# Kernel tuning notes

Measured on AMD Instinct MI355X. Metric: run time of the kernel, lower is better.

The kernel has to match this reference:

```python
import jax, jax.numpy as jnp
import numpy as np

B, L, D, DA, NL = 32, 2048, 512, 512, 512

def setup_inputs() -> dict:
    key = jax.random.key(0)
    k1, k2, k3, k4 = jax.random.split(key, 4)
    std = 0.03
    return {
        "x": jax.random.normal(k1, (B, L, D), dtype=jnp.float32),
        "W1": jax.random.normal(k2, (DA, D), dtype=jnp.float32) * std,   # first_linears[0].weight [d_a, size]
        "W2": jax.random.normal(k3, (NL, DA), dtype=jnp.float32) * std,  # second_linears[0].weight [n_labels, d_a]
        "W3": jax.random.normal(k4, (NL, D), dtype=jnp.float32) * std,   # third_linears[0].weight [n_labels, size]
        "b3": jnp.zeros((NL,), dtype=jnp.float32),                        # third_linears[0].bias
    }

def reference(x, W1, W2, W3, b3):
    # weights = tanh(first_linear(x)) : [B, L, DA]
    w = jnp.tanh(jnp.einsum("bld,ad->bla", x, W1))
    # att logits : [B, L, NL]; softmax over seq dim (dim=1), then transpose -> [B, NL, L]
    att = jax.nn.softmax(jnp.einsum("bla,na->bln", w, W2), axis=1)
    att_weights = jnp.swapaxes(att, 1, 2)  # [B, NL, L]
    # context_vector = att_weights @ x : [B, NL, D]
    context_vector = jnp.einsum("bnl,bld->bnd", att_weights, x)
    # label-wise diagonal mul-sum-add: [B, NL]
    weighted_output = jnp.einsum("bnd,nd->bn", context_vector, W3) + b3
    return (context_vector, weighted_output, att_weights)
```

## Files before the change

kernel.cpp:

```cpp
#include <hip/hip_runtime.h>
#include <math.h>

#define BB 32
#define LL 2048
#define DD 512
#define DA_ 512
#define NL_ 512

typedef __bf16 bf16;
typedef __bf16 bf16x8 __attribute__((ext_vector_type(8)));
typedef __bf16 bf16x4 __attribute__((ext_vector_type(4)));
typedef float floatx4 __attribute__((ext_vector_type(4)));

__device__ __forceinline__ void dma16(const void* g, void* l) {
    __builtin_amdgcn_global_load_lds((__attribute__((address_space(1))) void*)g,
                                     (__attribute__((address_space(3))) void*)l,
                                     16, 0, 0);
}

__device__ __forceinline__ float fast_tanh(float x) {
    const float e = __expf(2.f * x);
    return 1.f - 2.f * __builtin_amdgcn_rcpf(e + 1.f);
}

template <bool AF, bool BF>
__device__ __forceinline__ void gemm_core(const void* Ap_, const void* Bp_,
                                          int K, int lda, int ldb,
                                          floatx4 acc[4][4])
{
    __shared__ bf16 As[128 * 32];
    __shared__ bf16 Bs[128 * 32];
    const int tid = threadIdx.x;
    const int lane = tid & 63, wv = tid >> 6;
    const int wr = wv >> 1, wc = wv & 1;
    const int lm = lane & 15, quad = lane >> 4;

    for (int k0 = 0; k0 < K; k0 += 32) {
        __syncthreads();
        if constexpr (AF) {
            const float* A = (const float*)Ap_;
            #pragma unroll
            for (int it = 0; it < 4; ++it) {
                const int c = tid + it * 256;
                const int row = c >> 3, kq = c & 7;
                const float4 v = *(const float4*)(A + (size_t)row * lda + k0 + kq * 4);
                bf16x4 p = {(bf16)v.x, (bf16)v.y, (bf16)v.z, (bf16)v.w};
                *(bf16x4*)(As + row * 32 + kq * 4) = p;
            }
        } else {
            const bf16* A = (const bf16*)Ap_;
            #pragma unroll
            for (int it = 0; it < 2; ++it) {
                const int c = tid + it * 256;
                const int row = c >> 2, kq = c & 3;
                dma16(A + (size_t)row * lda + k0 + kq * 8, As + c * 8);
            }
        }
        if constexpr (BF) {
            const float* Bq = (const float*)Bp_;
            #pragma unroll
            for (int it = 0; it < 4; ++it) {
                const int c = tid + it * 256;
                const int row = c >> 3, kq = c & 7;
                const float4 v = *(const float4*)(Bq + (size_t)row * ldb + k0 + kq * 4);
                bf16x4 p = {(bf16)v.x, (bf16)v.y, (bf16)v.z, (bf16)v.w};
                *(bf16x4*)(Bs + row * 32 + kq * 4) = p;
            }
        } else {
            const bf16* Bq = (const bf16*)Bp_;
            #pragma unroll
            for (int it = 0; it < 2; ++it) {
                const int c = tid + it * 256;
                const int row = c >> 2, kq = c & 3;
                dma16(Bq + (size_t)row * ldb + k0 + kq * 8, Bs + c * 8);
            }
        }
        __syncthreads();

        bf16x8 af[4], bfr[4];
        #pragma unroll
        for (int t = 0; t < 4; ++t) {
            af[t]  = *(const bf16x8*)(As + (wr * 64 + t * 16 + lm) * 32 + quad * 8);
            bfr[t] = *(const bf16x8*)(Bs + (wc * 64 + t * 16 + lm) * 32 + quad * 8);
        }
        #pragma unroll
        for (int i = 0; i < 4; ++i)
            #pragma unroll
            for (int j = 0; j < 4; ++j)
                acc[i][j] = __builtin_amdgcn_mfma_f32_16x16x32_bf16(af[i], bfr[j], acc[i][j], 0, 0, 0);
    }
}


__global__ __launch_bounds__(256) void k_transpose(const float* __restrict__ x,
                                                   bf16* __restrict__ xT)
{
    __shared__ float T[64][68];
    const int b = blockIdx.z;
    const int l0 = blockIdx.x * 64, d0 = blockIdx.y * 64;
    const int tid = threadIdx.x;
    const float* xb = x + ((size_t)b * LL + l0) * DD + d0;
    #pragma unroll
    for (int it = 0; it < 4; ++it) {
        const int c = tid + it * 256;
        const int lr = c >> 4, cc = (c & 15) * 4;
        const float4 v = *(const float4*)(xb + (size_t)lr * DD + cc);
        T[lr][cc] = v.x; T[lr][cc + 1] = v.y; T[lr][cc + 2] = v.z; T[lr][cc + 3] = v.w;
    }
    __syncthreads();
    const int dl = tid >> 2, ls = (tid & 3) * 16;
    bf16x8 p0, p1;
    #pragma unroll
    for (int j = 0; j < 8; ++j) p0[j] = (bf16)T[ls + j][dl];
    #pragma unroll
    for (int j = 0; j < 8; ++j) p1[j] = (bf16)T[ls + 8 + j][dl];
    bf16* o = xT + ((size_t)b * DD + d0 + dl) * LL + l0 + ls;
    *(bf16x8*)o = p0;
    *(bf16x8*)(o + 8) = p1;
}

__global__ __launch_bounds__(256) void k_gemm1(const float* __restrict__ x,
                                               const float* __restrict__ W1,
                                               bf16* __restrict__ wb)
{
    const int n0 = blockIdx.x * 128;
    const size_t m0 = (size_t)blockIdx.y * 128;
    floatx4 acc[4][4];
    #pragma unroll
    for (int i = 0; i < 4; ++i)
        #pragma unroll
        for (int j = 0; j < 4; ++j) { floatx4 z = {0.f, 0.f, 0.f, 0.f}; acc[i][j] = z; }
    gemm_core<true, true>(x + m0 * DD, W1 + (size_t)n0 * DD, DD, DD, DD, acc);

    const int tid = threadIdx.x, lane = tid & 63, wv = tid >> 6;
    const int wr = wv >> 1, wc = wv & 1, lm = lane & 15, quad = lane >> 4;
    const size_t row0 = m0 + wr * 64 + quad * 4;
    const int col0 = n0 + wc * 64 + lm;
    #pragma unroll
    for (int i = 0; i < 4; ++i)
        #pragma unroll
        for (int j = 0; j < 4; ++j)
            #pragma unroll
            for (int r = 0; r < 4; ++r)
                wb[(row0 + i * 16 + r) * DA_ + col0 + j * 16] = (bf16)fast_tanh(acc[i][j][r]);
}

__global__ __launch_bounds__(256) void k_gemm2(const bf16* __restrict__ wb,
                                               const float* __restrict__ W2,
                                               float* __restrict__ att)
{
    const int c0 = blockIdx.x * 128;
    const int m0 = blockIdx.y * 128;
    floatx4 acc[4][4];
    #pragma unroll
    for (int i = 0; i < 4; ++i)
        #pragma unroll
        for (int j = 0; j < 4; ++j) { floatx4 z = {0.f, 0.f, 0.f, 0.f}; acc[i][j] = z; }
    gemm_core<true, false>(W2 + (size_t)m0 * DA_, wb + (size_t)c0 * DA_, DA_, DA_, DA_, acc);

    const int b = c0 >> 11, lloc = c0 & (LL - 1);
    const int tid = threadIdx.x, lane = tid & 63, wv = tid >> 6;
    const int wr = wv >> 1, wc = wv & 1, lm = lane & 15, quad = lane >> 4;
    float* base = att + ((size_t)b * NL_ + m0 + wr * 64 + quad * 4) * LL
                + lloc + wc * 64 + lm;
    #pragma unroll
    for (int i = 0; i < 4; ++i)
        #pragma unroll
        for (int j = 0; j < 4; ++j)
            #pragma unroll
            for (int r = 0; r < 4; ++r)
                base[(size_t)(i * 16 + r) * LL + j * 16] = acc[i][j][r];
}

__global__ __launch_bounds__(256) void k_softmax(float* __restrict__ att,
                                                 bf16* __restrict__ attb)
{
    const int tid = threadIdx.x;
    float* p = att + (size_t)blockIdx.x * LL;
    bf16* pb = attb + (size_t)blockIdx.x * LL;
    float4 v0 = *(const float4*)&p[tid * 4];
    float4 v1 = *(const float4*)&p[1024 + tid * 4];

    __shared__ float red[8];
    float m = fmaxf(fmaxf(fmaxf(v0.x, v0.y), fmaxf(v0.z, v0.w)),
                    fmaxf(fmaxf(v1.x, v1.y), fmaxf(v1.z, v1.w)));
    #pragma unroll
    for (int off = 32; off; off >>= 1) m = fmaxf(m, __shfl_down(m, off));
    if ((tid & 63) == 0) red[tid >> 6] = m;
    __syncthreads();
    m = fmaxf(fmaxf(red[0], red[1]), fmaxf(red[2], red[3]));

    v0.x = __expf(v0.x - m); v0.y = __expf(v0.y - m);
    v0.z = __expf(v0.z - m); v0.w = __expf(v0.w - m);
    v1.x = __expf(v1.x - m); v1.y = __expf(v1.y - m);
    v1.z = __expf(v1.z - m); v1.w = __expf(v1.w - m);
    float s = v0.x + v0.y + v0.z + v0.w + v1.x + v1.y + v1.z + v1.w;
    #pragma unroll
    for (int off = 32; off; off >>= 1) s += __shfl_down(s, off);
    if ((tid & 63) == 0) red[4 + (tid >> 6)] = s;
    __syncthreads();
    s = red[4] + red[5] + red[6] + red[7];

    const float inv = 1.0f / s;
    v0.x *= inv; v0.y *= inv; v0.z *= inv; v0.w *= inv;
    v1.x *= inv; v1.y *= inv; v1.z *= inv; v1.w *= inv;
    *(float4*)&p[tid * 4] = v0;
    *(float4*)&p[1024 + tid * 4] = v1;
    bf16x4 q0 = {(bf16)v0.x, (bf16)v0.y, (bf16)v0.z, (bf16)v0.w};
    bf16x4 q1 = {(bf16)v1.x, (bf16)v1.y, (bf16)v1.z, (bf16)v1.w};
    *(bf16x4*)(pb + tid * 4) = q0;
    *(bf16x4*)(pb + 1024 + tid * 4) = q1;
}

__global__ __launch_bounds__(256) void k_gemm3(const bf16* __restrict__ attb,
                                               const bf16* __restrict__ xT,
                                               float* __restrict__ ctx)
{
    const int b = blockIdx.z;
    const int n0 = blockIdx.x * 128;
    const int m0 = blockIdx.y * 128;
    floatx4 acc[4][4];
    #pragma unroll
    for (int i = 0; i < 4; ++i)
        #pragma unroll
        for (int j = 0; j < 4; ++j) { floatx4 z = {0.f, 0.f, 0.f, 0.f}; acc[i][j] = z; }
    gemm_core<false, false>(attb + ((size_t)b * NL_ + m0) * LL,
                            xT + ((size_t)b * DD + n0) * LL, LL, LL, LL, acc);

    const int tid = threadIdx.x, lane = tid & 63, wv = tid >> 6;
    const int wr = wv >> 1, wc = wv & 1, lm = lane & 15, quad = lane >> 4;
    float* base = ctx + ((size_t)b * NL_ + m0 + wr * 64 + quad * 4) * DD
                + n0 + wc * 64 + lm;
    #pragma unroll
    for (int i = 0; i < 4; ++i)
        #pragma unroll
        for (int j = 0; j < 4; ++j)
            #pragma unroll
            for (int r = 0; r < 4; ++r)
                base[(size_t)(i * 16 + r) * DD + j * 16] = acc[i][j][r];
}

__global__ __launch_bounds__(256) void k_wo(
    const float* __restrict__ ctx, const float* __restrict__ W3,
    const float* __restrict__ b3, float* __restrict__ wo)
{
    const int gw = blockIdx.x * 4 + (threadIdx.x >> 6);
    const int lane = threadIdx.x & 63;
    const int n = gw & (NL_ - 1);
    const float* c = ctx + (size_t)gw * DD;
    const float* w = W3 + (size_t)n * DD;
    float s = 0.f;
    #pragma unroll
    for (int it = 0; it < 2; ++it) {
        const float4 a = *(const float4*)&c[(it * 64 + lane) * 4];
        const float4 b = *(const float4*)&w[(it * 64 + lane) * 4];
        s += a.x * b.x + a.y * b.y + a.z * b.z + a.w * b.w;
    }
    #pragma unroll
    for (int off = 32; off; off >>= 1) s += __shfl_down(s, off);
    if (lane == 0) wo[gw] = s + b3[n];
}

extern "C" void kernel_launch(void* const* d_in, const int* in_sizes, int n_in,
                              void* d_out, int out_size, void* d_ws, size_t ws_size,
                              hipStream_t stream)
{
    const float* x  = (const float*)d_in[0];
    const float* W1 = (const float*)d_in[1];
    const float* W2 = (const float*)d_in[2];
    const float* W3 = (const float*)d_in[3];
    const float* b3 = (const float*)d_in[4];

    float* out = (float*)d_out;
    float* ctx = out;
    float* wo  = out + (size_t)BB * NL_ * DD;
    float* att = wo + (size_t)BB * NL_;

    bf16* xT = (bf16*)d_ws;
    bf16* wb = (bf16*)((char*)d_ws + (size_t)64 * 1024 * 1024);
    bf16* attb = wb;

    k_transpose<<<dim3(LL / 64, DD / 64, BB), 256, 0, stream>>>(x, xT);
    k_gemm1<<<dim3(DA_ / 128, (BB * LL) / 128), 256, 0, stream>>>(x, W1, wb);
    k_gemm2<<<dim3((BB * LL) / 128, NL_ / 128), 256, 0, stream>>>(wb, W2, att);
    k_softmax<<<BB * NL_, 256, 0, stream>>>(att, attb);
    k_gemm3<<<dim3(DD / 128, NL_ / 128, BB), 256, 0, stream>>>(attb, xT, ctx);
    k_wo<<<(BB * NL_) / 4, 256, 0, stream>>>(ctx, W3, b3, wo);
}
```

Measured before the change: 562.3 us.

## Pre-convert inputs to bf16 and store attention logits in bf16

Converts W1 and W2 to bf16 up front and has the transpose pass also emit a row-major bf16 copy of x. This lets all GEMMs use direct global-to-LDS DMA loads instead of fp32 loads with in-loop conversion. gemm2 now writes its logits as bf16, and softmax reads them, halving that intermediate traffic. The cost is extra small conversion launches, extra workspace, and lower logit precision before softmax.

```diff
diff --git a/kernel.cpp b/kernel.cpp
--- a/kernel.cpp
+++ b/kernel.cpp
@@ -23,8 +23,8 @@
     return 1.f - 2.f * __builtin_amdgcn_rcpf(e + 1.f);
 }
 
-template <bool AF, bool BF>
-__device__ __forceinline__ void gemm_core(const void* Ap_, const void* Bp_,
+__device__ __forceinline__ void gemm_core(const bf16* __restrict__ A,
+                                          const bf16* __restrict__ B,
                                           int K, int lda, int ldb,
                                           floatx4 acc[4][4])
 {
@@ -37,43 +37,17 @@
 
     for (int k0 = 0; k0 < K; k0 += 32) {
         __syncthreads();
-        if constexpr (AF) {
-            const float* A = (const float*)Ap_;
-            #pragma unroll
-            for (int it = 0; it < 4; ++it) {
-                const int c = tid + it * 256;
-                const int row = c >> 3, kq = c & 7;
-                const float4 v = *(const float4*)(A + (size_t)row * lda + k0 + kq * 4);
-                bf16x4 p = {(bf16)v.x, (bf16)v.y, (bf16)v.z, (bf16)v.w};
-                *(bf16x4*)(As + row * 32 + kq * 4) = p;
-            }
-        } else {
-            const bf16* A = (const bf16*)Ap_;
-            #pragma unroll
-            for (int it = 0; it < 2; ++it) {
-                const int c = tid + it * 256;
-                const int row = c >> 2, kq = c & 3;
-                dma16(A + (size_t)row * lda + k0 + kq * 8, As + c * 8);
-            }
+        #pragma unroll
+        for (int it = 0; it < 2; ++it) {
+            const int c = tid + it * 256;
+            const int row = c >> 2, kq = c & 3;
+            dma16(A + (size_t)row * lda + k0 + kq * 8, As + c * 8);
         }
-        if constexpr (BF) {
-            const float* Bq = (const float*)Bp_;
-            #pragma unroll
-            for (int it = 0; it < 4; ++it) {
-                const int c = tid + it * 256;
-                const int row = c >> 3, kq = c & 7;
-                const float4 v = *(const float4*)(Bq + (size_t)row * ldb + k0 + kq * 4);
-                bf16x4 p = {(bf16)v.x, (bf16)v.y, (bf16)v.z, (bf16)v.w};
-                *(bf16x4*)(Bs + row * 32 + kq * 4) = p;
-            }
-        } else {
-            const bf16* Bq = (const bf16*)Bp_;
-            #pragma unroll
-            for (int it = 0; it < 2; ++it) {
-                const int c = tid + it * 256;
-                const int row = c >> 2, kq = c & 3;
-                dma16(Bq + (size_t)row * ldb + k0 + kq * 8, Bs + c * 8);
-            }
+        #pragma unroll
+        for (int it = 0; it < 2; ++it) {
+            const int c = tid + it * 256;
+            const int row = c >> 2, kq = c & 3;
+            dma16(B + (size_t)row * ldb + k0 + kq * 8, Bs + c * 8);
         }
         __syncthreads();
 
@@ -91,21 +65,35 @@
     }
 }
 
+__global__ __launch_bounds__(256) void k_cvt(const float* __restrict__ src,
+                                             bf16* __restrict__ dst, int n)
+{
+    const int i = (blockIdx.x * 256 + threadIdx.x) * 4;
+    if (i < n) {
+        const float4 v = *(const float4*)(src + i);
+        bf16x4 p = {(bf16)v.x, (bf16)v.y, (bf16)v.z, (bf16)v.w};
+        *(bf16x4*)(dst + i) = p;
+    }
+}
 
 __global__ __launch_bounds__(256) void k_transpose(const float* __restrict__ x,
-                                                   bf16* __restrict__ xT)
+                                                   bf16* __restrict__ xT,
+                                                   bf16* __restrict__ xb)
 {
     __shared__ float T[64][68];
     const int b = blockIdx.z;
     const int l0 = blockIdx.x * 64, d0 = blockIdx.y * 64;
     const int tid = threadIdx.x;
-    const float* xb = x + ((size_t)b * LL + l0) * DD + d0;
+    const float* xsrc = x + ((size_t)b * LL + l0) * DD + d0;
+    bf16* xbdst = xb + ((size_t)b * LL + l0) * DD + d0;
     #pragma unroll
     for (int it = 0; it < 4; ++it) {
         const int c = tid + it * 256;
         const int lr = c >> 4, cc = (c & 15) * 4;
-        const float4 v = *(const float4*)(xb + (size_t)lr * DD + cc);
+        const float4 v = *(const float4*)(xsrc + (size_t)lr * DD + cc);
         T[lr][cc] = v.x; T[lr][cc + 1] = v.y; T[lr][cc + 2] = v.z; T[lr][cc + 3] = v.w;
+        bf16x4 p = {(bf16)v.x, (bf16)v.y, (bf16)v.z, (bf16)v.w};
+        *(bf16x4*)(xbdst + (size_t)lr * DD + cc) = p;
     }
     __syncthreads();
     const int dl = tid >> 2, ls = (tid & 3) * 16;
@@ -119,8 +107,8 @@
     *(bf16x8*)(o + 8) = p1;
 }
 
-__global__ __launch_bounds__(256) void k_gemm1(const float* __restrict__ x,
-                                               const float* __restrict__ W1,
+__global__ __launch_bounds__(256) void k_gemm1(const bf16* __restrict__ xb,
+                                               const bf16* __restrict__ W1b,
                                                bf16* __restrict__ wb)
 {
     const int n0 = blockIdx.x * 128;
@@ -130,7 +118,7 @@
     for (int i = 0; i < 4; ++i)
         #pragma unroll
         for (int j = 0; j < 4; ++j) { floatx4 z = {0.f, 0.f, 0.f, 0.f}; acc[i][j] = z; }
-    gemm_core<true, true>(x + m0 * DD, W1 + (size_t)n0 * DD, DD, DD, DD, acc);
+    gemm_core(xb + m0 * DD, W1b + (size_t)n0 * DD, DD, DD, DD, acc);
 
     const int tid = threadIdx.x, lane = tid & 63, wv = tid >> 6;
     const int wr = wv >> 1, wc = wv & 1, lm = lane & 15, quad = lane >> 4;
@@ -146,8 +134,8 @@
 }
 
 __global__ __launch_bounds__(256) void k_gemm2(const bf16* __restrict__ wb,
-                                               const float* __restrict__ W2,
-                                               float* __restrict__ att)
+                                               const bf16* __restrict__ W2b,
+                                               bf16* __restrict__ logitsb)
 {
     const int c0 = blockIdx.x * 128;
     const int m0 = blockIdx.y * 128;
@@ -156,45 +144,49 @@
     for (int i = 0; i < 4; ++i)
         #pragma unroll
         for (int j = 0; j < 4; ++j) { floatx4 z = {0.f, 0.f, 0.f, 0.f}; acc[i][j] = z; }
-    gemm_core<true, false>(W2 + (size_t)m0 * DA_, wb + (size_t)c0 * DA_, DA_, DA_, DA_, acc);
+    gemm_core(W2b + (size_t)m0 * DA_, wb + (size_t)c0 * DA_, DA_, DA_, DA_, acc);
 
     const int b = c0 >> 11, lloc = c0 & (LL - 1);
     const int tid = threadIdx.x, lane = tid & 63, wv = tid >> 6;
     const int wr = wv >> 1, wc = wv & 1, lm = lane & 15, quad = lane >> 4;
-    float* base = att + ((size_t)b * NL_ + m0 + wr * 64 + quad * 4) * LL
-                + lloc + wc * 64 + lm;
+    bf16* base = logitsb + ((size_t)b * NL_ + m0 + wr * 64 + quad * 4) * LL
+               + lloc + wc * 64 + lm;
     #pragma unroll
     for (int i = 0; i < 4; ++i)
         #pragma unroll
         for (int j = 0; j < 4; ++j)
             #pragma unroll
             for (int r = 0; r < 4; ++r)
-                base[(size_t)(i * 16 + r) * LL + j * 16] = acc[i][j][r];
-}
-
-__global__ __launch_bounds__(256) void k_softmax(float* __restrict__ att,
+                base[(size_t)(i * 16 + r) * LL + j * 16] = (bf16)acc[i][j][r];
+}
+
+__global__ __launch_bounds__(256) void k_softmax(const bf16* __restrict__ logitsb,
+                                                 float* __restrict__ att,
                                                  bf16* __restrict__ attb)
 {
     const int tid = threadIdx.x;
-    float* p = att + (size_t)blockIdx.x * LL;
+    const bf16* p = logitsb + (size_t)blockIdx.x * LL;
+    float* po = att + (size_t)blockIdx.x * LL;
     bf16* pb = attb + (size_t)blockIdx.x * LL;
-    float4 v0 = *(const float4*)&p[tid * 4];
-    float4 v1 = *(const float4*)&p[1024 + tid * 4];
+
+    const bf16x8 v = *(const bf16x8*)(p + tid * 8);
+    float f[8];
+    #pragma unroll
+    for (int j = 0; j < 8; ++j) f[j] = (float)v[j];
 
     __shared__ float red[8];
-    float m = fmaxf(fmaxf(fmaxf(v0.x, v0.y), fmaxf(v0.z, v0.w)),
-                    fmaxf(fmaxf(v1.x, v1.y), fmaxf(v1.z, v1.w)));
+    float m = f[0];
+    #pragma unroll
+    for (int j = 1; j < 8; ++j) m = fmaxf(m, f[j]);
     #pragma unroll
     for (int off = 32; off; off >>= 1) m = fmaxf(m, __shfl_down(m, off));
     if ((tid & 63) == 0) red[tid >> 6] = m;
     __syncthreads();
     m = fmaxf(fmaxf(red[0], red[1]), fmaxf(red[2], red[3]));
 
-    v0.x = __expf(v0.x - m); v0.y = __expf(v0.y - m);
-    v0.z = __expf(v0.z - m); v0.w = __expf(v0.w - m);
-    v1.x = __expf(v1.x - m); v1.y = __expf(v1.y - m);
-    v1.z = __expf(v1.z - m); v1.w = __expf(v1.w - m);
-    float s = v0.x + v0.y + v0.z + v0.w + v1.x + v1.y + v1.z + v1.w;
+    float s = 0.f;
+    #pragma unroll
+    for (int j = 0; j < 8; ++j) { f[j] = __expf(f[j] - m); s += f[j]; }
     #pragma unroll
     for (int off = 32; off; off >>= 1) s += __shfl_down(s, off);
     if ((tid & 63) == 0) red[4 + (tid >> 6)] = s;
@@ -202,14 +194,14 @@
     s = red[4] + red[5] + red[6] + red[7];
 
     const float inv = 1.0f / s;
-    v0.x *= inv; v0.y *= inv; v0.z *= inv; v0.w *= inv;
-    v1.x *= inv; v1.y *= inv; v1.z *= inv; v1.w *= inv;
-    *(float4*)&p[tid * 4] = v0;
-    *(float4*)&p[1024 + tid * 4] = v1;
-    bf16x4 q0 = {(bf16)v0.x, (bf16)v0.y, (bf16)v0.z, (bf16)v0.w};
-    bf16x4 q1 = {(bf16)v1.x, (bf16)v1.y, (bf16)v1.z, (bf16)v1.w};
-    *(bf16x4*)(pb + tid * 4) = q0;
-    *(bf16x4*)(pb + 1024 + tid * 4) = q1;
+    float4 o0, o1;
+    o0.x = f[0] * inv; o0.y = f[1] * inv; o0.z = f[2] * inv; o0.w = f[3] * inv;
+    o1.x = f[4] * inv; o1.y = f[5] * inv; o1.z = f[6] * inv; o1.w = f[7] * inv;
+    *(float4*)(po + tid * 8) = o0;
+    *(float4*)(po + tid * 8 + 4) = o1;
+    bf16x8 q = {(bf16)o0.x, (bf16)o0.y, (bf16)o0.z, (bf16)o0.w,
+                (bf16)o1.x, (bf16)o1.y, (bf16)o1.z, (bf16)o1.w};
+    *(bf16x8*)(pb + tid * 8) = q;
 }
 
 __global__ __launch_bounds__(256) void k_gemm3(const bf16* __restrict__ attb,
@@ -224,8 +216,8 @@
     for (int i = 0; i < 4; ++i)
         #pragma unroll
         for (int j = 0; j < 4; ++j) { floatx4 z = {0.f, 0.f, 0.f, 0.f}; acc[i][j] = z; }
-    gemm_core<false, false>(attb + ((size_t)b * NL_ + m0) * LL,
-                            xT + ((size_t)b * DD + n0) * LL, LL, LL, LL, acc);
+    gemm_core(attb + ((size_t)b * NL_ + m0) * LL,
+              xT + ((size_t)b * DD + n0) * LL, LL, LL, LL, acc);
 
     const int tid = threadIdx.x, lane = tid & 63, wv = tid >> 6;
     const int wr = wv >> 1, wc = wv & 1, lm = lane & 15, quad = lane >> 4;
@@ -276,14 +268,22 @@
     float* wo  = out + (size_t)BB * NL_ * DD;
     float* att = wo + (size_t)BB * NL_;
 
-    bf16* xT = (bf16*)d_ws;
-    bf16* wb = (bf16*)((char*)d_ws + (size_t)64 * 1024 * 1024);
-    bf16* attb = wb;
-
-    k_transpose<<<dim3(LL / 64, DD / 64, BB), 256, 0, stream>>>(x, xT);
-    k_gemm1<<<dim3(DA_ / 128, (BB * LL) / 128), 256, 0, stream>>>(x, W1, wb);
-    k_gemm2<<<dim3((BB * LL) / 128, NL_ / 128), 256, 0, stream>>>(wb, W2, att);
-    k_softmax<<<BB * NL_, 256, 0, stream>>>(att, attb);
+    char* wsp = (char*)d_ws;
+    const size_t M64 = (size_t)64 * 1024 * 1024;
+    bf16* xT      = (bf16*)(wsp);
+    bf16* xb      = (bf16*)(wsp + M64);
+    bf16* logitsb = (bf16*)(wsp + M64);
+    bf16* wb      = (bf16*)(wsp + 2 * M64);
+    bf16* attb    = (bf16*)(wsp + 2 * M64);
+    bf16* W1b     = (bf16*)(wsp + 3 * M64);
+    bf16* W2b     = W1b + (size_t)DA_ * DD;
+
+    k_cvt<<<(DA_ * DD) / 1024, 256, 0, stream>>>(W1, W1b, DA_ * DD);
+    k_cvt<<<(NL_ * DA_) / 1024, 256, 0, stream>>>(W2, W2b, NL_ * DA_);
+    k_transpose<<<dim3(LL / 64, DD / 64, BB), 256, 0, stream>>>(x, xT, xb);
+    k_gemm1<<<dim3(DA_ / 128, (BB * LL) / 128), 256, 0, stream>>>(xb, W1b, wb);
+    k_gemm2<<<dim3((BB * LL) / 128, NL_ / 128), 256, 0, stream>>>(wb, W2b, logitsb);
+    k_softmax<<<BB * NL_, 256, 0, stream>>>(logitsb, att, attb);
     k_gemm3<<<dim3(DD / 128, NL_ / 128, BB), 256, 0, stream>>>(attb, xT, ctx);
     k_wo<<<(BB * NL_) / 4, 256, 0, stream>>>(ctx, W3, b3, wo);
 }
```

After: 524.4 us. 6.7% less time.
